# Optimization experiments

Hardware: AMD Instinct MI355X
Metric: run time of the kernel (lower is better)

The kernel has to match this reference:

```python
import jax, jax.numpy as jnp
import numpy as np

D_MODEL, D_STATE, D_CONV, EXPAND, N_HEADS = 768, 64, 4, 2, 12
D_INNER = D_MODEL * EXPAND           # 1536
HEAD_DIM = D_INNER // N_HEADS        # 128
IN_PROJ = D_INNER * 2 + N_HEADS * D_STATE * 2 + N_HEADS  # 4620
EPS = 1e-5


def setup_inputs() -> dict:
    key = jax.random.key(0)
    ks = jax.random.split(key, 8)
    s = lambda fan_in: 1.0 / np.sqrt(fan_in)
    return {
        "x": jax.random.normal(ks[0], (1, 1024, D_MODEL), dtype=jnp.float32),
        "W_in": jax.random.normal(ks[1], (IN_PROJ, D_MODEL), dtype=jnp.float32) * s(D_MODEL),
        "conv_w": jax.random.normal(ks[2], (D_INNER, D_CONV), dtype=jnp.float32) * s(D_CONV),
        "conv_b": jnp.zeros((D_INNER,), dtype=jnp.float32),
        "A_log": jnp.full((N_HEADS,), np.log(0.5), dtype=jnp.float32),
        "Dp": jnp.ones((N_HEADS,), dtype=jnp.float32),
        "dt_bias": jnp.zeros((N_HEADS,), dtype=jnp.float32),
        "W_out": jax.random.normal(ks[3], (D_MODEL, D_INNER), dtype=jnp.float32) * s(D_INNER),
        "norm_w": jnp.ones((D_INNER,), dtype=jnp.float32),
    }


def _causal_conv1d(x, w, b):
    # x: (B,L,Din), depthwise causal conv with kernel size D_CONV
    L = x.shape[1]
    xp = jnp.pad(x, ((0, 0), (D_CONV - 1, 0), (0, 0)))
    y = b
    for i in range(D_CONV):  # fixed small kernel, unrolled
        y = y + xp[:, i:i + L, :] * w[:, i]
    return y


def reference(x, W_in, conv_w, conv_b, A_log, Dp, dt_bias, W_out, norm_w):
    B_sz, L, _ = x.shape
    nh, ds, hd = N_HEADS, D_STATE, HEAD_DIM
    proj = jnp.einsum('bld,pd->blp', x, W_in)
    z = proj[:, :, :D_INNER]
    x_ssm = proj[:, :, D_INNER:2 * D_INNER]
    o = 2 * D_INNER
    Bm = proj[:, :, o:o + nh * ds].reshape(B_sz, L, nh, ds)
    Cm = proj[:, :, o + nh * ds:o + 2 * nh * ds].reshape(B_sz, L, nh, ds)
    dt_r = proj[:, :, o + 2 * nh * ds:]
    dt = jax.nn.softplus(dt_r) + dt_bias[None, None, :]          # (B,L,nh)

    x_ssm = jax.nn.silu(_causal_conv1d(x_ssm, conv_w, conv_b))
    x_ssm = x_ssm.reshape(B_sz, L, nh, hd)

    A = -jnp.exp(A_log)                                          # (nh,)
    log_decay = A[None, None, :] * dt                            # (B,L,nh)
    Phi = jnp.cumsum(log_decay, axis=1)
    dB = dt[..., None] * Bm                                      # (B,L,nh,ds)
    # b: (B,L,nh,hd,ds) outer product
    b = dB[:, :, :, None, :] * x_ssm[..., None]
    max_exp = 80.0
    exp_neg_Phi = jnp.exp(jnp.minimum(-Phi, max_exp))[..., None, None]
    b_cumsum = jnp.cumsum(exp_neg_Phi * b, axis=1)
    h = jnp.exp(Phi)[..., None, None] * b_cumsum                 # (B,L,nh,hd,ds)
    y = jnp.sum(Cm[:, :, :, None, :] * h, axis=-1)               # (B,L,nh,hd)
    y = y + Dp[None, None, :, None] * x_ssm
    y = y.reshape(B_sz, L, D_INNER)

    # RMSNorm then gate
    rms = jax.lax.rsqrt(jnp.mean(y * y, axis=-1, keepdims=True) + EPS)
    y = y * rms * norm_w
    y = y * jax.nn.silu(z)
    return jnp.einsum('bli,di->bld', y, W_out)
```

## Files before the change

kernel.cpp:

```cpp
#include <hip/hip_runtime.h>
#include <cmath>

#define LSEQ   1024
#define NPROJ  4620
#define NPADW  4736
#define DINNER 1536
#define NH     12
#define HDIM   128
#define OFF_Z  0
#define OFF_X  1536
#define OFF_B  3072
#define OFF_C  3840
#define OFF_DT 4608

typedef unsigned short u16;
typedef unsigned int u32;
typedef short bf16x8 __attribute__((ext_vector_type(8)));
typedef float f32x4 __attribute__((ext_vector_type(4)));

__device__ inline u16 f2b(float f) {
  unsigned u = __float_as_uint(f);
  return (u16)((u + 0x7fffu + ((u >> 16) & 1u)) >> 16);
}
__device__ inline float b2f(u16 h) { return __uint_as_float(((unsigned)h) << 16); }
__device__ inline u32 pk2(float a, float b) { return (u32)f2b(a) | ((u32)f2b(b) << 16); }

__device__ inline void gll16(const void* g, void* l) {
  __builtin_amdgcn_global_load_lds((const __attribute__((address_space(1))) void*)g,
                                   (__attribute__((address_space(3))) void*)l, 16, 0, 0);
}

#define S0N 196608
#define S1N 909312
#define S1V 887040
#define S2N 294912
__global__ __launch_bounds__(256) void ksplit_all(const float* __restrict__ x,
    const float* __restrict__ Wi, const float* __restrict__ Wo,
    u16* __restrict__ Ah, u16* __restrict__ Wh, u16* __restrict__ Woh) {
  int i = blockIdx.x * 256 + threadIdx.x;
  const float* src; u16* hi; int j, valid;
  if (i < S0N)            { src = x;  hi = Ah;  j = i;              valid = S0N; }
  else if (i < S0N + S1N) { src = Wi; hi = Wh;  j = i - S0N;        valid = S1V; }
  else                    { src = Wo; hi = Woh; j = i - S0N - S1N;  valid = S2N; }
  float4 v = (j < valid) ? ((const float4*)src)[j] : make_float4(0.f, 0.f, 0.f, 0.f);
  ((uint2*)hi)[j] = make_uint2(pk2(v.x, v.y), pk2(v.z, v.w));
}

template<int BM, int BN, int MAP, bool NG>
__global__ __launch_bounds__(256) void gemm1(const u16* __restrict__ Ah,
    const u16* __restrict__ Wh, float* __restrict__ C,
    int lda, int ldw, int Ksl, int Nreal, int ldc) {
  constexpr int PLA = BM * 64;
  constexpr int IA = BM / 8, IW = BN / 8, ITOT = IA + IW;
  constexpr int FRn = BN / 32;
  __shared__ u16 lds[PLA + BN * 64];
  const int tid = threadIdx.x;
  const int l = tid & 63, w = tid >> 6;
  const int wm = w >> 1, wn = w & 1;
  const int kg = l >> 4, li = l & 15;

  int b = blockIdx.x, m0, n0, koff;
  float* Cp = C;
  if (MAP == 0) {
    int xcd = b & 7, idx = b >> 3;
    m0 = (idx & 15) * 64;
    n0 = (xcd * 5 + (idx >> 4)) * 128;
    koff = 0;
    if (NG && n0 >= NPADW) return;
  } else {
    int xcd = b & 7, idx = b >> 3;
    int gg = xcd * 6 + (idx >> 4);
    m0 = (idx & 15) * 64;
    n0 = (gg % 12) * 64;
    koff = (gg / 12) * 384;
    Cp = C + (size_t)(gg / 12) * LSEQ * ldc;
  }

  const int srcg = ((l & 7) ^ (l >> 3)) * 8;
  auto stage = [&](int t) {
    const int k0 = koff + t * 64;
    for (int q = w; q < ITOT; q += 4) {
      const u16* gb; int r0b, ldk, dst;
      if (q < IA) { gb = Ah; r0b = m0 + 8 * q;        dst = 8 * q * 64;              ldk = lda; }
      else        { gb = Wh; r0b = n0 + 8 * (q - IA); dst = PLA + 8 * (q - IA) * 64; ldk = ldw; }
      gll16(gb + (size_t)(r0b + (l >> 3)) * ldk + k0 + srcg, &lds[dst]);
    }
  };
  auto rd = [&](int region, int row, int ks) -> bf16x8 {
    return *(const bf16x8*)&lds[region + row * 64 + (((ks * 4 + kg) ^ (row & 7)) << 3)];
  };

  f32x4 acc[2][FRn];
#pragma unroll
  for (int m = 0; m < 2; ++m)
#pragma unroll
    for (int n = 0; n < FRn; ++n) acc[m][n] = (f32x4){0.f, 0.f, 0.f, 0.f};

  const int NT = Ksl / 64;
  stage(0);
  asm volatile("s_waitcnt vmcnt(0)" ::: "memory");
  __syncthreads();
  for (int t = 0; t < NT; ++t) {
    bf16x8 af[2][2], wf[FRn][2];
#pragma unroll
    for (int ks = 0; ks < 2; ++ks) {
#pragma unroll
      for (int m = 0; m < 2; ++m)
        af[m][ks] = rd(0, wm * 32 + m * 16 + li, ks);
#pragma unroll
      for (int n = 0; n < FRn; ++n)
        wf[n][ks] = rd(PLA, wn * (BN / 2) + n * 16 + li, ks);
    }
    __syncthreads();
    if (t + 1 < NT) stage(t + 1);
#pragma unroll
    for (int ks = 0; ks < 2; ++ks)
#pragma unroll
      for (int m = 0; m < 2; ++m)
#pragma unroll
        for (int n = 0; n < FRn; ++n)
          acc[m][n] = __builtin_amdgcn_mfma_f32_16x16x32_bf16(af[m][ks], wf[n][ks], acc[m][n], 0, 0, 0);
    if (t + 1 < NT) {
      asm volatile("s_waitcnt vmcnt(0)" ::: "memory");
      __syncthreads();
    }
  }
#pragma unroll
  for (int m = 0; m < 2; ++m) {
    int rbase = m0 + wm * 32 + m * 16 + kg * 4;
#pragma unroll
    for (int n = 0; n < FRn; ++n) {
      int col = n0 + wn * (BN / 2) + n * 16 + li;
      if (!NG || col < Nreal) {
#pragma unroll
        for (int r = 0; r < 4; ++r)
          Cp[(size_t)(rbase + r) * ldc + col] = acc[m][n][r];
      }
    }
  }
}

__global__ __launch_bounds__(256) void addk(const float* __restrict__ P,
    float* __restrict__ out) {
  const int S = LSEQ * 768 / 4;
  int i = blockIdx.x * 256 + threadIdx.x;
  float4 a = ((const float4*)P)[i];
  float4 b = ((const float4*)P)[i + S];
  float4 c = ((const float4*)P)[i + 2 * S];
  float4 d = ((const float4*)P)[i + 3 * S];
  ((float4*)out)[i] = make_float4(a.x + b.x + c.x + d.x, a.y + b.y + c.y + d.y,
                                  a.z + b.z + c.z + d.z, a.w + b.w + c.w + d.w);
}

__global__ __launch_bounds__(256) void dtphi(const float* __restrict__ proj,
    const float* __restrict__ A_log, const float* __restrict__ dt_bias,
    float* __restrict__ Phi, float* __restrict__ dts) {
  int h = blockIdx.x, tid = threadIdx.x;
  float Ac = -expf(A_log[h]);
  float bb = dt_bias[h];
  float v[4], s = 0.f;
#pragma unroll
  for (int u = 0; u < 4; ++u) {
    int t = tid * 4 + u;
    float xr = proj[(size_t)t * NPROJ + OFF_DT + h];
    float sp = (xr > 20.f) ? xr : log1pf(expf(xr));
    v[u] = sp + bb;
    s += v[u];
  }
  int lane = tid & 63, wv = tid >> 6;
  float ps = s;
#pragma unroll
  for (int d = 1; d < 64; d <<= 1) {
    float o = __shfl_up(ps, d);
    if (lane >= d) ps += o;
  }
  __shared__ float wsum[4];
  if (lane == 63) wsum[wv] = ps;
  __syncthreads();
  float off = 0.f;
  for (int w = 0; w < wv; ++w) off += wsum[w];
  float run = off + ps - s;
#pragma unroll
  for (int u = 0; u < 4; ++u) {
    int t = tid * 4 + u;
    run += v[u];
    Phi[t * NH + h] = Ac * run;
    dts[t * NH + h] = v[u];
  }
}

__global__ __launch_bounds__(256) void conv_state(const float* __restrict__ proj,
    const float* __restrict__ cw, const float* __restrict__ cb,
    const float* __restrict__ Phi, const float* __restrict__ dts,
    u16* __restrict__ xactT, float* __restrict__ SlocF) {
  const int k = blockIdx.x, h = blockIdx.y, tid = threadIdx.x;
  const int l = tid & 63, w = tid >> 6, kg = l >> 4, li = l & 15;
  __shared__ u16 Bw[64 * 64];
  __shared__ u16 Xt[128 * 64];
  __shared__ float wS[64];
  const int s0 = k * 64;
  if (tid < 64) {
    float pe = Phi[(s0 + 63) * NH + h];
    float p  = Phi[(s0 + tid) * NH + h];
    wS[tid] = expf(pe + fminf(-p, 80.f)) * dts[(s0 + tid) * NH + h];
  }
  __syncthreads();
#pragma unroll
  for (int u = 0; u < 4; ++u) {
    int idx = tid + u * 256, s = idx >> 4, q = (idx & 15) * 4;
    float4 v = *(const float4*)(proj + (size_t)(s0 + s) * NPROJ + OFF_B + h * 64 + q);
    float ws_ = wS[s];
    float vv[4] = {v.x, v.y, v.z, v.w};
#pragma unroll
    for (int j = 0; j < 4; ++j) {
      int d = q + j;
      Bw[d * 64 + (((s >> 3) ^ (d & 7)) << 3) + (s & 7)] = f2b(vv[j] * ws_);
    }
  }
  {
    int c = tid & 127, th = tid >> 7;
    int cg = h * HDIM + c;
    float w0 = cw[cg * 4], w1 = cw[cg * 4 + 1], w2 = cw[cg * 4 + 2], w3 = cw[cg * 4 + 3];
    float bias = cb[cg];
    int tb = s0 + th * 32;
    auto P = [&](int t) { return (t >= 0) ? proj[(size_t)t * NPROJ + OFF_X + cg] : 0.f; };
    float x0 = P(tb - 3), x1 = P(tb - 2), x2 = P(tb - 1);
    u32 pkb[16];
    float prev = 0.f;
#pragma unroll
    for (int i = 0; i < 32; ++i) {
      float x3 = P(tb + i);
      float a = bias;
      a = fmaf(x0, w0, a); a = fmaf(x1, w1, a); a = fmaf(x2, w2, a); a = fmaf(x3, w3, a);
      float sv = a / (1.f + expf(-a));
      if (i & 1) pkb[i >> 1] = pk2(prev, sv); else prev = sv;
      x0 = x1; x1 = x2; x2 = x3;
    }
#pragma unroll
    for (int g = 0; g < 4; ++g) {
      int sg = th * 4 + g;
      *(uint4*)&Xt[c * 64 + ((sg ^ (c & 7)) << 3)] =
          make_uint4(pkb[g * 4], pkb[g * 4 + 1], pkb[g * 4 + 2], pkb[g * 4 + 3]);
    }
    size_t xo = ((size_t)(k * NH + h) * 128 + c) * 64 + th * 32;
#pragma unroll
    for (int g = 0; g < 4; ++g)
      *(uint4*)(xactT + xo + g * 8) =
          make_uint4(pkb[g * 4], pkb[g * 4 + 1], pkb[g * 4 + 2], pkb[g * 4 + 3]);
  }
  __syncthreads();
  const int wm = w >> 1, wn = w & 1;
  auto rd = [&](const u16* reg, int row, int ks) -> bf16x8 {
    return *(const bf16x8*)&reg[row * 64 + (((ks * 4 + kg) ^ (row & 7)) << 3)];
  };
  f32x4 acc[4][2];
#pragma unroll
  for (int m = 0; m < 4; ++m)
#pragma unroll
    for (int n = 0; n < 2; ++n) acc[m][n] = (f32x4){0.f, 0.f, 0.f, 0.f};
#pragma unroll
  for (int ks = 0; ks < 2; ++ks) {
    bf16x8 xf[4], bf[2];
#pragma unroll
    for (int m = 0; m < 4; ++m) xf[m] = rd(Xt, wm * 64 + m * 16 + li, ks);
#pragma unroll
    for (int n = 0; n < 2; ++n) bf[n] = rd(Bw, wn * 32 + n * 16 + li, ks);
#pragma unroll
    for (int m = 0; m < 4; ++m)
#pragma unroll
      for (int n = 0; n < 2; ++n)
        acc[m][n] = __builtin_amdgcn_mfma_f32_16x16x32_bf16(xf[m], bf[n], acc[m][n], 0, 0, 0);
  }
  float* dst = SlocF + ((size_t)(k * NH + h) << 13);
#pragma unroll
  for (int m = 0; m < 4; ++m)
#pragma unroll
    for (int n = 0; n < 2; ++n)
#pragma unroll
      for (int r = 0; r < 4; ++r) {
        int c = wm * 64 + m * 16 + kg * 4 + r;
        int d = wn * 32 + n * 16 + li;
        dst[c * 64 + d] = acc[m][n][r];
      }
}

__global__ __launch_bounds__(256) void chunk_scan(const float* __restrict__ SlocF,
    u16* __restrict__ SlocT, const float* __restrict__ Phi) {
  int b = blockIdx.x;
  int h = b >> 5;
  int e = (b & 31) * 256 + threadIdx.x;
  float run = SlocF[((size_t)h << 13) + e];
  SlocT[((size_t)h << 13) + e] = f2b(run);
#pragma unroll
  for (int k = 1; k < 16; ++k) {
    float lam = expf(Phi[(k * 64 + 63) * NH + h] - Phi[(k * 64 - 1) * NH + h]);
    size_t o = ((size_t)(k * NH + h) << 13) + e;
    run = fmaf(lam, run, SlocF[o]);
    SlocT[o] = f2b(run);
  }
}

__global__ __launch_bounds__(256) void ssm_out(const float* __restrict__ proj,
    const u16* __restrict__ xactT, const float* __restrict__ Phi,
    const float* __restrict__ dts, const float* __restrict__ Dp,
    const u16* __restrict__ SlocT, u16* __restrict__ ybuf) {
  const int k = blockIdx.x, h = blockIdx.y, zh = blockIdx.z, tid = threadIdx.x;
  const int l = tid & 63, w = tid >> 6, kg = l >> 4, li = l & 15;
  const int wm = w >> 1, wn = w & 1;
  __shared__ u16 Cs[4096], Bs[4096], Ps[4096], Xs[4096], Ss[4096];
  __shared__ float phiT[64], eSs[64], dSs[64], eTs[64];
  const int t0 = k * 64;
  const int srcg = ((l & 7) ^ (l >> 3)) * 8;
  {
    const u16* xsrc = xactT + ((size_t)(k * NH + h) * 128 + zh * 64) * 64;
#pragma unroll
    for (int j = 0; j < 2; ++j) {
      int rb = w * 16 + j * 8;
      gll16(xsrc + (size_t)(rb + (l >> 3)) * 64 + srcg, &Xs[rb * 64]);
    }
    if (k > 0) {
      const u16* ssrc = SlocT + (((size_t)((k - 1) * NH + h)) << 13) + (size_t)(zh * 64) * 64;
#pragma unroll
      for (int j = 0; j < 2; ++j) {
        int rb = w * 16 + j * 8;
        gll16(ssrc + (size_t)(rb + (l >> 3)) * 64 + srcg, &Ss[rb * 64]);
      }
    }
  }
#pragma unroll
  for (int u = 0; u < 4; ++u) {
    int idx = tid + u * 256, i = idx >> 4, q = (idx & 15) * 4;
    int aoff = i * 64 + (((q >> 3) ^ (i & 7)) << 3) + (q & 4);
    float4 cv = *(const float4*)(proj + (size_t)(t0 + i) * NPROJ + OFF_C + h * 64 + q);
    float4 bv = *(const float4*)(proj + (size_t)(t0 + i) * NPROJ + OFF_B + h * 64 + q);
    *(uint2*)&Cs[aoff] = make_uint2(pk2(cv.x, cv.y), pk2(cv.z, cv.w));
    *(uint2*)&Bs[aoff] = make_uint2(pk2(bv.x, bv.y), pk2(bv.z, bv.w));
  }
  if (tid < 64) {
    float p = Phi[(t0 + tid) * NH + h];
    phiT[tid] = p;
    eSs[tid] = fminf(-p, 80.f);
    dSs[tid] = dts[(t0 + tid) * NH + h];
    eTs[tid] = (k > 0) ? expf(p - Phi[(t0 - 1) * NH + h]) : 0.f;
  }
  __syncthreads();
  auto rd = [&](const u16* reg, int row, int ks) -> bf16x8 {
    return *(const bf16x8*)&reg[row * 64 + (((ks * 4 + kg) ^ (row & 7)) << 3)];
  };
  bf16x8 Cf[2][2];
  f32x4 accS[2][2];
#pragma unroll
  for (int m = 0; m < 2; ++m)
#pragma unroll
    for (int n = 0; n < 2; ++n) accS[m][n] = (f32x4){0.f, 0.f, 0.f, 0.f};
#pragma unroll
  for (int ks = 0; ks < 2; ++ks) {
    bf16x8 Bf[2];
#pragma unroll
    for (int m = 0; m < 2; ++m) Cf[m][ks] = rd(Cs, wm * 32 + m * 16 + li, ks);
#pragma unroll
    for (int n = 0; n < 2; ++n) Bf[n] = rd(Bs, wn * 32 + n * 16 + li, ks);
#pragma unroll
    for (int m = 0; m < 2; ++m)
#pragma unroll
      for (int n = 0; n < 2; ++n)
        accS[m][n] = __builtin_amdgcn_mfma_f32_16x16x32_bf16(Cf[m][ks], Bf[n], accS[m][n], 0, 0, 0);
  }
#pragma unroll
  for (int m = 0; m < 2; ++m)
#pragma unroll
    for (int n = 0; n < 2; ++n)
#pragma unroll
      for (int r = 0; r < 4; ++r) {
        int t = wm * 32 + m * 16 + kg * 4 + r;
        int s = wn * 32 + n * 16 + li;
        float f = (s <= t) ? expf(phiT[t] + eSs[s]) * dSs[s] : 0.f;
        Ps[t * 64 + (((s >> 3) ^ (t & 7)) << 3) + (s & 7)] = f2b(accS[m][n][r] * f);
      }
  __syncthreads();
  f32x4 accY[2][2], acc2[2][2];
#pragma unroll
  for (int m = 0; m < 2; ++m)
#pragma unroll
    for (int n = 0; n < 2; ++n) {
      accY[m][n] = (f32x4){0.f, 0.f, 0.f, 0.f};
      acc2[m][n] = (f32x4){0.f, 0.f, 0.f, 0.f};
    }
#pragma unroll
  for (int ks = 0; ks < 2; ++ks) {
    bf16x8 Pf[2], Xf[2];
#pragma unroll
    for (int m = 0; m < 2; ++m) Pf[m] = rd(Ps, wm * 32 + m * 16 + li, ks);
#pragma unroll
    for (int n = 0; n < 2; ++n) Xf[n] = rd(Xs, wn * 32 + n * 16 + li, ks);
#pragma unroll
    for (int m = 0; m < 2; ++m)
#pragma unroll
      for (int n = 0; n < 2; ++n)
        accY[m][n] = __builtin_amdgcn_mfma_f32_16x16x32_bf16(Pf[m], Xf[n], accY[m][n], 0, 0, 0);
    if (k > 0) {
      bf16x8 Sf[2];
#pragma unroll
      for (int n = 0; n < 2; ++n) Sf[n] = rd(Ss, wn * 32 + n * 16 + li, ks);
#pragma unroll
      for (int m = 0; m < 2; ++m)
#pragma unroll
        for (int n = 0; n < 2; ++n)
          acc2[m][n] = __builtin_amdgcn_mfma_f32_16x16x32_bf16(Cf[m][ks], Sf[n], acc2[m][n], 0, 0, 0);
    }
  }
  float dp = Dp[h];
#pragma unroll
  for (int m = 0; m < 2; ++m)
#pragma unroll
    for (int n = 0; n < 2; ++n)
#pragma unroll
      for (int r = 0; r < 4; ++r) {
        int t = wm * 32 + m * 16 + kg * 4 + r;
        int c = wn * 32 + n * 16 + li;
        float xv = b2f(Xs[c * 64 + (((t >> 3) ^ (c & 7)) << 3) + (t & 7)]);
        float val = accY[m][n][r] + eTs[t] * acc2[m][n][r] + dp * xv;
        ybuf[(size_t)(t0 + t) * DINNER + h * HDIM + zh * 64 + c] = f2b(val);
      }
}

__global__ __launch_bounds__(256) void norm_gate(const u16* __restrict__ y,
    const float* __restrict__ proj, const float* __restrict__ nw,
    u16* __restrict__ yh) {
  int t = blockIdx.x, tid = threadIdx.x;
  float v[6], ss = 0.f;
#pragma unroll
  for (int k = 0; k < 6; ++k) {
    v[k] = b2f(y[(size_t)t * DINNER + tid + k * 256]);
    ss = fmaf(v[k], v[k], ss);
  }
#pragma unroll
  for (int d = 1; d < 64; d <<= 1) ss += __shfl_xor(ss, d);
  __shared__ float wsum[4];
  int wv = tid >> 6;
  if ((tid & 63) == 0) wsum[wv] = ss;
  __syncthreads();
  float tot = wsum[0] + wsum[1] + wsum[2] + wsum[3];
  float rms = rsqrtf(tot / 1536.f + 1e-5f);
#pragma unroll
  for (int k = 0; k < 6; ++k) {
    int c = tid + k * 256;
    float z = proj[(size_t)t * NPROJ + OFF_Z + c];
    float sz = z / (1.f + expf(-z));
    yh[(size_t)t * DINNER + c] = f2b(v[k] * rms * nw[c] * sz);
  }
}

extern "C" void kernel_launch(void* const* d_in, const int* in_sizes, int n_in,
                              void* d_out, int out_size, void* d_ws, size_t ws_size,
                              hipStream_t stream) {
  const float* x       = (const float*)d_in[0];
  const float* W_in    = (const float*)d_in[1];
  const float* conv_w  = (const float*)d_in[2];
  const float* conv_b  = (const float*)d_in[3];
  const float* A_log   = (const float*)d_in[4];
  const float* Dp      = (const float*)d_in[5];
  const float* dt_bias = (const float*)d_in[6];
  const float* W_out   = (const float*)d_in[7];
  const float* norm_w  = (const float*)d_in[8];
  float* out = (float*)d_out;

  char* base = (char*)d_ws;
  size_t o = 0;
  auto alloc = [&](size_t bytes) { char* r = base + o; o += (bytes + 255) & ~(size_t)255; return r; };
  float* proj  = (float*)alloc((size_t)LSEQ * NPROJ * 4);
  u16*   ybuf  = (u16*)alloc((size_t)LSEQ * DINNER * 2);
  float* Phi   = (float*)alloc((size_t)LSEQ * NH * 4);
  float* dtsb  = (float*)alloc((size_t)LSEQ * NH * 4);
  float* SlocF = (float*)alloc((size_t)16 * NH * 8192 * 4);
  u16*   SlocT = (u16*)alloc((size_t)16 * NH * 8192 * 2);
  u16*   xactT = (u16*)alloc((size_t)16 * NH * 128 * 64 * 2);
  u16* Ah  = (u16*)alloc((size_t)LSEQ * 768 * 2);
  u16* Wh  = (u16*)alloc((size_t)NPADW * 768 * 2);
  u16* Woh = (u16*)alloc((size_t)768 * DINNER * 2);
  u16* Yh  = (u16*)alloc((size_t)LSEQ * DINNER * 2);
  float* Pp = proj;

  ksplit_all<<<dim3((S0N + S1N + S2N) / 256), 256, 0, stream>>>(
      x, W_in, W_out, Ah, Wh, Woh);
  gemm1<64, 128, 0, true><<<dim3(640), 256, 0, stream>>>(
      Ah, Wh, proj, 768, 768, 768, NPROJ, NPROJ);
  dtphi<<<dim3(NH), 256, 0, stream>>>(proj, A_log, dt_bias, Phi, dtsb);
  conv_state<<<dim3(16, NH), 256, 0, stream>>>(proj, conv_w, conv_b, Phi, dtsb, xactT, SlocF);
  chunk_scan<<<dim3(NH * 32), 256, 0, stream>>>(SlocF, SlocT, Phi);
  ssm_out<<<dim3(16, NH, 2), 256, 0, stream>>>(proj, xactT, Phi, dtsb, Dp, SlocT, ybuf);
  norm_gate<<<dim3(LSEQ), 256, 0, stream>>>(ybuf, proj, norm_w, Yh);
  gemm1<64, 64, 1, false><<<dim3(768), 256, 0, stream>>>(
      Yh, Woh, Pp, 1536, 1536, 384, 768, 768);
  addk<<<dim3(LSEQ * 768 / 4 / 256), 256, 0, stream>>>(Pp, out);
}
```

Baseline: 72.25 us.

## Fuse RMSNorm and gating into ssm_out, defer rms scaling to final reduction

Removes the separate norm_gate kernel. ssm_out now applies norm weight and SiLU(z) gating directly and accumulates per-token sum of squares into a global buffer with atomics. The rms factor is applied after the out-projection in the split-K reduction kernel, which is valid because the per-token scale is linear through the GEMM. The split-K partials also get their own buffer instead of reusing proj. This saves one launch and a bf16 round trip of y, at the cost of atomics and extra z loads inside ssm_out.

```diff
diff --git a/kernel.cpp b/kernel.cpp
--- a/kernel.cpp
+++ b/kernel.cpp
@@ -51,7 +51,7 @@
     const u16* __restrict__ Wh, float* __restrict__ C,
     int lda, int ldw, int Ksl, int Nreal, int ldc) {
   constexpr int PLA = BM * 64;
-  constexpr int IA = BM / 8, IW = BN / 8, ITOT = IA + IW;
+  constexpr int IA = BM / 8, ITOT = IA + BN / 8;
   constexpr int FRn = BN / 32;
   __shared__ u16 lds[PLA + BN * 64];
   const int tid = threadIdx.x;
@@ -141,21 +141,26 @@
 }
 
 __global__ __launch_bounds__(256) void addk(const float* __restrict__ P,
-    float* __restrict__ out) {
+    const float* __restrict__ rmsacc, float* __restrict__ out) {
   const int S = LSEQ * 768 / 4;
   int i = blockIdx.x * 256 + threadIdx.x;
+  int t = i / 192;
+  float rms = rsqrtf(rmsacc[t] * (1.f / 1536.f) + 1e-5f);
   float4 a = ((const float4*)P)[i];
   float4 b = ((const float4*)P)[i + S];
   float4 c = ((const float4*)P)[i + 2 * S];
   float4 d = ((const float4*)P)[i + 3 * S];
-  ((float4*)out)[i] = make_float4(a.x + b.x + c.x + d.x, a.y + b.y + c.y + d.y,
-                                  a.z + b.z + c.z + d.z, a.w + b.w + c.w + d.w);
+  ((float4*)out)[i] = make_float4((a.x + b.x + c.x + d.x) * rms,
+                                  (a.y + b.y + c.y + d.y) * rms,
+                                  (a.z + b.z + c.z + d.z) * rms,
+                                  (a.w + b.w + c.w + d.w) * rms);
 }
 
 __global__ __launch_bounds__(256) void dtphi(const float* __restrict__ proj,
     const float* __restrict__ A_log, const float* __restrict__ dt_bias,
-    float* __restrict__ Phi, float* __restrict__ dts) {
+    float* __restrict__ Phi, float* __restrict__ dts, float* __restrict__ rmsacc) {
   int h = blockIdx.x, tid = threadIdx.x;
+  if (h < 4) rmsacc[h * 256 + tid] = 0.f;
   float Ac = -expf(A_log[h]);
   float bb = dt_bias[h];
   float v[4], s = 0.f;
@@ -195,8 +200,8 @@
     u16* __restrict__ xactT, float* __restrict__ SlocF) {
   const int k = blockIdx.x, h = blockIdx.y, tid = threadIdx.x;
   const int l = tid & 63, w = tid >> 6, kg = l >> 4, li = l & 15;
-  __shared__ u16 Bw[64 * 64];
-  __shared__ u16 Xt[128 * 64];
+  __shared__ u16 Bw[4096];
+  __shared__ u16 Xt[8192];
   __shared__ float wS[64];
   const int s0 = k * 64;
   if (tid < 64) {
@@ -271,7 +276,7 @@
       for (int n = 0; n < 2; ++n)
         acc[m][n] = __builtin_amdgcn_mfma_f32_16x16x32_bf16(xf[m], bf[n], acc[m][n], 0, 0, 0);
   }
-  float* dst = SlocF + ((size_t)(k * NH + h) << 13);
+  float* dst = SlocF + (((size_t)(k * NH + h)) << 13);
 #pragma unroll
   for (int m = 0; m < 4; ++m)
 #pragma unroll
@@ -303,23 +308,24 @@
 __global__ __launch_bounds__(256) void ssm_out(const float* __restrict__ proj,
     const u16* __restrict__ xactT, const float* __restrict__ Phi,
     const float* __restrict__ dts, const float* __restrict__ Dp,
-    const u16* __restrict__ SlocT, u16* __restrict__ ybuf) {
+    const u16* __restrict__ SlocT, const float* __restrict__ nw,
+    u16* __restrict__ Yh, float* __restrict__ rmsacc) {
   const int k = blockIdx.x, h = blockIdx.y, zh = blockIdx.z, tid = threadIdx.x;
   const int l = tid & 63, w = tid >> 6, kg = l >> 4, li = l & 15;
   const int wm = w >> 1, wn = w & 1;
   __shared__ u16 Cs[4096], Bs[4096], Ps[4096], Xs[4096], Ss[4096];
   __shared__ float phiT[64], eSs[64], dSs[64], eTs[64];
+  __shared__ float sq[64], nws[64];
   const int t0 = k * 64;
   const int srcg = ((l & 7) ^ (l >> 3)) * 8;
   {
-    const u16* xsrc = xactT + ((size_t)(k * NH + h) * 128 + zh * 64) * 64;
 #pragma unroll
     for (int j = 0; j < 2; ++j) {
       int rb = w * 16 + j * 8;
-      gll16(xsrc + (size_t)(rb + (l >> 3)) * 64 + srcg, &Xs[rb * 64]);
+      gll16(xactT + ((size_t)(k * NH + h) * 128 + zh * 64 + rb + (l >> 3)) * 64 + srcg, &Xs[rb * 64]);
     }
     if (k > 0) {
-      const u16* ssrc = SlocT + (((size_t)((k - 1) * NH + h)) << 13) + (size_t)(zh * 64) * 64;
+      const u16* ssrc = SlocT + (((size_t)((k - 1) * NH + h) * 128 + zh * 64)) * 64;
 #pragma unroll
       for (int j = 0; j < 2; ++j) {
         int rb = w * 16 + j * 8;
@@ -342,6 +348,8 @@
     eSs[tid] = fminf(-p, 80.f);
     dSs[tid] = dts[(t0 + tid) * NH + h];
     eTs[tid] = (k > 0) ? expf(p - Phi[(t0 - 1) * NH + h]) : 0.f;
+    sq[tid] = 0.f;
+    nws[tid] = nw[h * HDIM + zh * 64 + tid];
   }
   __syncthreads();
   auto rd = [&](const u16* reg, int row, int ks) -> bf16x8 {
@@ -410,6 +418,7 @@
     }
   }
   float dp = Dp[h];
+  float ls[8] = {};
 #pragma unroll
   for (int m = 0; m < 2; ++m)
 #pragma unroll
@@ -420,35 +429,20 @@
         int c = wn * 32 + n * 16 + li;
         float xv = b2f(Xs[c * 64 + (((t >> 3) ^ (c & 7)) << 3) + (t & 7)]);
         float val = accY[m][n][r] + eTs[t] * acc2[m][n][r] + dp * xv;
-        ybuf[(size_t)(t0 + t) * DINNER + h * HDIM + zh * 64 + c] = f2b(val);
+        ls[m * 4 + r] = fmaf(val, val, ls[m * 4 + r]);
+        float z = proj[(size_t)(t0 + t) * NPROJ + OFF_Z + h * HDIM + zh * 64 + c];
+        float sz = z / (1.f + expf(-z));
+        Yh[(size_t)(t0 + t) * DINNER + h * HDIM + zh * 64 + c] = f2b(val * nws[c] * sz);
       }
-}
-
-__global__ __launch_bounds__(256) void norm_gate(const u16* __restrict__ y,
-    const float* __restrict__ proj, const float* __restrict__ nw,
-    u16* __restrict__ yh) {
-  int t = blockIdx.x, tid = threadIdx.x;
-  float v[6], ss = 0.f;
-#pragma unroll
-  for (int k = 0; k < 6; ++k) {
-    v[k] = b2f(y[(size_t)t * DINNER + tid + k * 256]);
-    ss = fmaf(v[k], v[k], ss);
-  }
-#pragma unroll
-  for (int d = 1; d < 64; d <<= 1) ss += __shfl_xor(ss, d);
-  __shared__ float wsum[4];
-  int wv = tid >> 6;
-  if ((tid & 63) == 0) wsum[wv] = ss;
-  __syncthreads();
-  float tot = wsum[0] + wsum[1] + wsum[2] + wsum[3];
-  float rms = rsqrtf(tot / 1536.f + 1e-5f);
-#pragma unroll
-  for (int k = 0; k < 6; ++k) {
-    int c = tid + k * 256;
-    float z = proj[(size_t)t * NPROJ + OFF_Z + c];
-    float sz = z / (1.f + expf(-z));
-    yh[(size_t)t * DINNER + c] = f2b(v[k] * rms * nw[c] * sz);
-  }
+#pragma unroll
+  for (int j = 0; j < 8; ++j) {
+    float v = ls[j];
+    v += __shfl_xor(v, 1); v += __shfl_xor(v, 2);
+    v += __shfl_xor(v, 4); v += __shfl_xor(v, 8);
+    if (li == 0) atomicAdd(&sq[wm * 32 + (j >> 2) * 16 + kg * 4 + (j & 3)], v);
+  }
+  __syncthreads();
+  if (tid < 64) atomicAdd(&rmsacc[t0 + tid], sq[tid]);
 }
 
 extern "C" void kernel_launch(void* const* d_in, const int* in_sizes, int n_in,
@@ -468,29 +462,29 @@
   char* base = (char*)d_ws;
   size_t o = 0;
   auto alloc = [&](size_t bytes) { char* r = base + o; o += (bytes + 255) & ~(size_t)255; return r; };
-  float* proj  = (float*)alloc((size_t)LSEQ * NPROJ * 4);
-  u16*   ybuf  = (u16*)alloc((size_t)LSEQ * DINNER * 2);
-  float* Phi   = (float*)alloc((size_t)LSEQ * NH * 4);
-  float* dtsb  = (float*)alloc((size_t)LSEQ * NH * 4);
-  float* SlocF = (float*)alloc((size_t)16 * NH * 8192 * 4);
-  u16*   SlocT = (u16*)alloc((size_t)16 * NH * 8192 * 2);
-  u16*   xactT = (u16*)alloc((size_t)16 * NH * 128 * 64 * 2);
-  u16* Ah  = (u16*)alloc((size_t)LSEQ * 768 * 2);
-  u16* Wh  = (u16*)alloc((size_t)NPADW * 768 * 2);
-  u16* Woh = (u16*)alloc((size_t)768 * DINNER * 2);
-  u16* Yh  = (u16*)alloc((size_t)LSEQ * DINNER * 2);
-  float* Pp = proj;
+  float* proj   = (float*)alloc((size_t)LSEQ * NPROJ * 4);
+  float* Phi    = (float*)alloc((size_t)LSEQ * NH * 4);
+  float* dts    = (float*)alloc((size_t)LSEQ * NH * 4);
+  float* rmsacc = (float*)alloc((size_t)LSEQ * 4);
+  float* SlocF  = (float*)alloc((size_t)16 * NH * 8192 * 4);
+  u16*   SlocT  = (u16*)alloc((size_t)16 * NH * 8192 * 2);
+  u16*   xactT  = (u16*)alloc((size_t)16 * NH * 8192 * 2);
+  u16*   Ah     = (u16*)alloc((size_t)LSEQ * 768 * 2);
+  u16*   Wh     = (u16*)alloc((size_t)NPADW * 768 * 2);
+  u16*   Woh    = (u16*)alloc((size_t)768 * DINNER * 2);
+  u16*   Yh     = (u16*)alloc((size_t)LSEQ * DINNER * 2);
+  float* Pp     = (float*)alloc((size_t)4 * LSEQ * 768 * 4);
 
   ksplit_all<<<dim3((S0N + S1N + S2N) / 256), 256, 0, stream>>>(
       x, W_in, W_out, Ah, Wh, Woh);
   gemm1<64, 128, 0, true><<<dim3(640), 256, 0, stream>>>(
       Ah, Wh, proj, 768, 768, 768, NPROJ, NPROJ);
-  dtphi<<<dim3(NH), 256, 0, stream>>>(proj, A_log, dt_bias, Phi, dtsb);
-  conv_state<<<dim3(16, NH), 256, 0, stream>>>(proj, conv_w, conv_b, Phi, dtsb, xactT, SlocF);
+  dtphi<<<dim3(NH), 256, 0, stream>>>(proj, A_log, dt_bias, Phi, dts, rmsacc);
+  conv_state<<<dim3(16, NH), 256, 0, stream>>>(proj, conv_w, conv_b, Phi, dts, xactT, SlocF);
   chunk_scan<<<dim3(NH * 32), 256, 0, stream>>>(SlocF, SlocT, Phi);
-  ssm_out<<<dim3(16, NH, 2), 256, 0, stream>>>(proj, xactT, Phi, dtsb, Dp, SlocT, ybuf);
-  norm_gate<<<dim3(LSEQ), 256, 0, stream>>>(ybuf, proj, norm_w, Yh);
+  ssm_out<<<dim3(16, NH, 2), 256, 0, stream>>>(
+      proj, xactT, Phi, dts, Dp, SlocT, norm_w, Yh, rmsacc);
   gemm1<64, 64, 1, false><<<dim3(768), 256, 0, stream>>>(
       Yh, Woh, Pp, 1536, 1536, 384, 768, 768);
-  addk<<<dim3(LSEQ * 768 / 4 / 256), 256, 0, stream>>>(Pp, out);
-}
+  addk<<<dim3(LSEQ * 768 / 4 / 256), 256, 0, stream>>>(Pp, rmsacc, out);
+}
```

Result: faster. 69.34 us (-4.0%).
